# Kernel optimization log

Measured on AMD Instinct MI355X. Metric: run time of the kernel, lower is better.

The kernel has to match this reference:

```python
import jax, jax.numpy as jnp
from jax import lax
import numpy as np

N, BITS, NCLS = 2048, 64, 100
LAMBDA = 1.0
ALPHA = 1.0


def setup_inputs() -> dict:
    key = jax.random.key(0)
    ku, kl = jax.random.split(key)
    u = jax.random.normal(ku, (N, BITS), dtype=jnp.float32)
    labels = jax.random.randint(kl, (N,), 0, NCLS)
    y = jax.nn.one_hot(labels, NCLS, dtype=jnp.float32)  # [N, C]
    return {"u": u, "y": y}


def reference(u, y):
    # inner_product[i, j] = <u_i, u_j>;  s[i, j] = (y_i . y_j > 0)
    ip = u @ u.T                      # [N, N]
    s = (y @ y.T) > 0                 # [N, N] bool

    def step(carry, xs):
        tot, cnt = carry
        ip_row, s_row = xs            # [N], [N]
        pos = s_row
        neg = ~s_row
        # triple[p, n] = ip[p] - ip[n] - ALPHA, clamped like the original
        T = jnp.clip(ip_row[:, None] - ip_row[None, :] - ALPHA, -100.0, 50.0)
        # -(T - log(1 + exp(T))) = softplus(T) - T
        L = jax.nn.softplus(T) - T    # [N, N]
        pm = (pos[:, None] & neg[None, :]).astype(L.dtype)
        npairs = pm.sum()
        valid = (pos.sum() > 0) & (neg.sum() > 0)
        row_loss = jnp.where(valid, (L * pm).sum() / jnp.maximum(npairs, 1.0), 0.0)
        return (tot + row_loss, cnt + valid.astype(jnp.float32)), None

    (tot, cnt), _ = lax.scan(step, (jnp.float32(0.0), jnp.float32(0.0)), (ip, s))
    loss1 = jnp.where(cnt > 0, tot / jnp.maximum(cnt, 1.0), 0.0)
    loss2 = LAMBDA * jnp.mean((u - jnp.sign(u)) ** 2)
    return loss1 + loss2
```

## Files before the change

kernel.cpp:

```cpp
#include <hip/hip_runtime.h>
#include <hip/hip_bf16.h>
#include <math.h>

#define NROWS 2048
#define BITS  64
#define NCLS  100
#define ALPHA_C  1.0f
#define LAMBDA_C 1.0f
#define ECLAMP   1.0e9f
#define NPMAX    64
#define EPS      20

typedef __bf16 bf16x8 __attribute__((ext_vector_type(8)));
typedef float  floatx4 __attribute__((ext_vector_type(4)));


__device__ __forceinline__ float block_reduce_sum(float v, float* wsum) {
    __syncthreads();
    #pragma unroll
    for (int off = 32; off > 0; off >>= 1) v += __shfl_down(v, off);
    int tid = threadIdx.x;
    if ((tid & 63) == 0) wsum[tid >> 6] = v;
    __syncthreads();
    float r = 0.f;
    if (tid == 0) {
        #pragma unroll
        for (int w = 0; w < 4; ++w) r += wsum[w];
    }
    return r;
}

__device__ __forceinline__ float softplus_mt(float T) {
    return fmaxf(-T, 0.f) + __logf(1.f + __expf(-fabsf(T)));
}


__global__ __launch_bounds__(256) void prep_kernel(const float* __restrict__ u,
                                                   const float* __restrict__ y,
                                                   unsigned short* __restrict__ ub,
                                                   unsigned char* __restrict__ lab8,
                                                   float* __restrict__ qp,
                                                   float* __restrict__ rl) {
    const int tid = threadIdx.x;
    if (blockIdx.x < 64) {
        __shared__ float wsum[4];
        const int base = blockIdx.x * 2048 + tid * 8;
        float4 v0 = *(const float4*)(u + base);
        float4 v1 = *(const float4*)(u + base + 4);
        float vv[8] = {v0.x, v0.y, v0.z, v0.w, v1.x, v1.y, v1.z, v1.w};
        unsigned short ob[8];
        float q = 0.f;
        #pragma unroll
        for (int m = 0; m < 8; ++m) {
            const float v = vv[m];
            const float sg = (v > 0.f) ? 1.f : ((v < 0.f) ? -1.f : 0.f);
            const float d = v - sg;
            q = fmaf(d, d, q);
            __hip_bfloat16 h = __float2bfloat16(v);
            ob[m] = *reinterpret_cast<unsigned short*>(&h);
        }
        *(uint4*)(ub + base) = *(const uint4*)ob;
        float t = block_reduce_sum(q, wsum);
        if (tid == 0) qp[blockIdx.x] = t;
    } else {
        const int bi = blockIdx.x - 64;
        if (tid == 0) ((float4*)rl)[bi] = make_float4(0.f, 0.f, 0.f, 0.f);
        const int row = bi * 4 + (tid >> 6);
        const int lane = tid & 63;
        const float* yr = y + (size_t)row * NCLS;
        float v0 = yr[lane];
        float v1 = (lane < NCLS - 64) ? yr[lane + 64] : 0.f;
        unsigned long long m0 = __ballot(v0 > 0.5f);
        unsigned long long m1 = __ballot(v1 > 0.5f);
        if (lane == 0) {
            int c = m0 ? (__ffsll(m0) - 1) : (m1 ? 64 + __ffsll(m1) - 1 : 0);
            lab8[row] = (unsigned char)c;
        }
    }
}

__global__ __launch_bounds__(256) void posk_kernel(const float* __restrict__ u,
                                                   const unsigned char* __restrict__ lab8,
                                                   float* __restrict__ Ep,
                                                   int* __restrict__ npg) {
    __shared__ unsigned char labL[NROWS];
    __shared__ float uloc[4][BITS];
    __shared__ int   lstJ[4][NPMAX];
    const int tid = threadIdx.x;
    const int wave = tid >> 6;
    const int lane = tid & 63;
    const int row = blockIdx.x * 4 + wave;

    ((uint2*)labL)[tid] = ((const uint2*)lab8)[tid];
    uloc[wave][lane] = u[(size_t)row * BITS + lane];
    __syncthreads();

    const int ci = labL[row];
    int np = 0;
    const unsigned long long mylt = (lane == 63) ? ~0ull >> 1
                                                 : ((1ull << (lane + 1)) - 1) >> 1;
    #pragma unroll 4
    for (int m = 0; m < NROWS / 64; ++m) {
        const int j = m * 64 + lane;
        const bool match = (labL[j] == ci);
        unsigned long long bal = __ballot(match);
        if (bal) {
            if (match) {
                const unsigned long long below = (lane == 0) ? 0ull : (bal << (64 - lane));
                const int slot = np + __popcll(below);
                if (slot < NPMAX) lstJ[wave][slot] = j;
            }
            np += __popcll(bal);
        }
    }
    const int npc = (np < NPMAX) ? np : NPMAX;

    float val = 0.f;
    if (lane < npc) {
        const int j = lstJ[wave][lane];
        const float4* uj4 = (const float4*)(u + (size_t)j * BITS);
        float s0 = 0.f, s1 = 0.f, s2 = 0.f, s3 = 0.f;
        #pragma unroll
        for (int kk = 0; kk < BITS / 4; ++kk) {
            float4 vj = uj4[kk];
            s0 = fmaf(vj.x, uloc[wave][4 * kk + 0], s0);
            s1 = fmaf(vj.y, uloc[wave][4 * kk + 1], s1);
            s2 = fmaf(vj.z, uloc[wave][4 * kk + 2], s2);
            s3 = fmaf(vj.w, uloc[wave][4 * kk + 3], s3);
        }
        val = fminf(__expf(-((s0 + s1) + (s2 + s3))), ECLAMP);
    }
    Ep[(size_t)row * NPMAX + lane] = val;
    if (lane == 0) npg[row] = np;
}

__global__ __launch_bounds__(256, 4) void evalj2_kernel(const unsigned short* __restrict__ ub,
                                                        const unsigned char* __restrict__ lab8,
                                                        const float* __restrict__ Ep,
                                                        const int* __restrict__ npg,
                                                        float* __restrict__ rl) {
    __shared__ unsigned char labL[NROWS];
    __shared__ float epT[NPMAX][EPS];
    __shared__ int np16[16];
    __shared__ float wsum[16][4];

    const int tid  = threadIdx.x;
    const int wave = tid >> 6;
    const int lane = tid & 63;
    const int rsel = lane & 15;
    const int quad = lane >> 4;
    const int koff = quad * 8;
    const int i0    = (blockIdx.x >> 3) * 16;
    const int jbase = (blockIdx.x & 7) * 256;

    ((uint2*)labL)[tid] = ((const uint2*)lab8)[tid];
    #pragma unroll
    for (int it = 0; it < 4; ++it) {
        const int idx = tid + it * 256;
        const int r = idx >> 6, k = idx & 63;
        epT[k][r] = Ep[(size_t)(i0 + r) * NPMAX + k];
    }
    if (tid < 16) np16[tid] = npg[i0 + tid];

    uint4 a0r = *(const uint4*)(ub + (size_t)(i0 + rsel) * BITS + koff);
    uint4 a1r = *(const uint4*)(ub + (size_t)(i0 + rsel) * BITS + 32 + koff);
    bf16x8 A0 = __builtin_bit_cast(bf16x8, a0r);
    bf16x8 A1 = __builtin_bit_cast(bf16x8, a1r);

    float Eb[4][4];
    int colj[4];
    #pragma unroll
    for (int t = 0; t < 4; ++t) {
        const int j0 = jbase + (wave * 4 + t) * 16;
        const int jr = j0 + rsel;
        colj[t] = jr;
        uint4 b0r = *(const uint4*)(ub + (size_t)jr * BITS + koff);
        uint4 b1r = *(const uint4*)(ub + (size_t)jr * BITS + 32 + koff);
        bf16x8 B0 = __builtin_bit_cast(bf16x8, b0r);
        bf16x8 B1 = __builtin_bit_cast(bf16x8, b1r);
        floatx4 c = {0.f, 0.f, 0.f, 0.f};
        c = __builtin_amdgcn_mfma_f32_16x16x32_bf16(A0, B0, c, 0, 0, 0);
        c = __builtin_amdgcn_mfma_f32_16x16x32_bf16(A1, B1, c, 0, 0, 0);
        #pragma unroll
        for (int r = 0; r < 4; ++r) {
            const int rowLab = labL[i0 + 4 * quad + r];
            const int colLab = labL[jr];
            Eb[t][r] = (colLab == rowLab) ? 0.f
                                          : fminf(__expf(c[r] + ALPHA_C), ECLAMP);
        }
    }
    __syncthreads();

    int npmx = 0;
    #pragma unroll
    for (int r = 0; r < 16; ++r) {
        int n = np16[r]; n = (n > NPMAX) ? NPMAX : n;
        npmx = (n > npmx) ? n : npmx;
    }
    const int npr = (npmx + 1) & ~1;

    float s[4] = {0.f, 0.f, 0.f, 0.f};
    for (int k = 0; k < npr; k += 2) {
        const float4 e0 = *(const float4*)(&epT[k][4 * quad]);
        const float4 e1 = *(const float4*)(&epT[k + 1][4 * quad]);
        const float e0v[4] = {e0.x, e0.y, e0.z, e0.w};
        const float e1v[4] = {e1.x, e1.y, e1.z, e1.w};
        #pragma unroll
        for (int t = 0; t < 4; ++t) {
            #pragma unroll
            for (int r = 0; r < 4; ++r) {
                const float q0 = Eb[t][r];
                const float f = fmaf(q0, e0v[r], 1.f);
                const float g = fmaf(q0, e1v[r], 1.f);
                s[r] += __log2f(f * g);
            }
        }
    }

    #pragma unroll
    for (int r = 0; r < 4; ++r) {
        #pragma unroll
        for (int off = 1; off < 16; off <<= 1) s[r] += __shfl_xor(s[r], off);
    }
    if (rsel == 0) {
        #pragma unroll
        for (int r = 0; r < 4; ++r) wsum[4 * quad + r][wave] = s[r];
    }
    __syncthreads();
    if (tid < 16) {
        const float ln2 = 0.6931471805599453f;
        const float tot = ((wsum[tid][0] + wsum[tid][1]) +
                           (wsum[tid][2] + wsum[tid][3])) * ln2;
        atomicAdd(&rl[i0 + tid], tot);
    }
}

__global__ __launch_bounds__(256) void finalize3_kernel(const float* __restrict__ rl,
                                                        const int* __restrict__ npg,
                                                        const float* __restrict__ qp,
                                                        float* __restrict__ out) {
    __shared__ float wsum[4];
    const int tid = threadIdx.x;
    float t = 0.f, v = 0.f;
    for (int row = tid; row < NROWS; row += 256) {
        const int np = npg[row];
        const int nneg = NROWS - np;
        const int valid = (np > 0 && nneg > 0) ? 1 : 0;
        t += valid ? (rl[row] / fmaxf((float)np * (float)nneg, 1.f)) : 0.f;
        v += (float)valid;
    }
    float q = (tid < 64) ? qp[tid] : 0.f;
    float tt = block_reduce_sum(t, wsum);
    float vv = block_reduce_sum(v, wsum);
    float qq = block_reduce_sum(q, wsum);
    if (tid == 0) {
        const float loss1 = (vv > 0.f) ? (tt / fmaxf(vv, 1.f)) : 0.f;
        const float loss2 = LAMBDA_C * (qq / (float)(NROWS * BITS));
        out[0] = loss1 + loss2;
    }
}


__global__ __launch_bounds__(256) void labels_only_kernel(const float* __restrict__ y,
                                                          int* __restrict__ labels) {
    const int tid = threadIdx.x;
    const int row = blockIdx.x * 4 + (tid >> 6);
    const int lane = tid & 63;
    const float* yr = y + (size_t)row * NCLS;
    float v0 = yr[lane];
    float v1 = (lane < NCLS - 64) ? yr[lane + 64] : 0.f;
    unsigned long long m0 = __ballot(v0 > 0.5f);
    unsigned long long m1 = __ballot(v1 > 0.5f);
    if (lane == 0) {
        int c = m0 ? (__ffsll(m0) - 1) : (m1 ? 64 + __ffsll(m1) - 1 : 0);
        labels[row] = c;
    }
}

__global__ __launch_bounds__(256) void row_loss_kernel(const float* __restrict__ u,
                                                       const int* __restrict__ labels,
                                                       float* __restrict__ acc) {
    __shared__ float a[NROWS];
    __shared__ float apv[NROWS];
    __shared__ int lab[NROWS];
    __shared__ float ui[BITS];
    __shared__ int npos_s;
    __shared__ float wsum[4];

    const int i = blockIdx.x;
    const int tid = threadIdx.x;

    if (tid < BITS) ui[tid] = u[(size_t)i * BITS + tid];
    if (tid == 0) npos_s = 0;
    __syncthreads();

    #pragma unroll
    for (int m = 0; m < NROWS / 256; ++m) {
        const int j = tid + m * 256;
        const float4* uj = (const float4*)(u + (size_t)j * BITS);
        float s0 = 0.f, s1 = 0.f, s2 = 0.f, s3 = 0.f;
        #pragma unroll
        for (int q = 0; q < BITS / 4; ++q) {
            float4 v = uj[q];
            s0 = fmaf(v.x, ui[4 * q + 0], s0);
            s1 = fmaf(v.y, ui[4 * q + 1], s1);
            s2 = fmaf(v.z, ui[4 * q + 2], s2);
            s3 = fmaf(v.w, ui[4 * q + 3], s3);
        }
        a[j] = (s0 + s1) + (s2 + s3);
        lab[j] = labels[j];
    }
    __syncthreads();

    const int c = lab[i];
    #pragma unroll
    for (int m = 0; m < NROWS / 256; ++m) {
        const int j = tid + m * 256;
        if (lab[j] == c) { int k = atomicAdd(&npos_s, 1); apv[k] = a[j]; }
    }
    __syncthreads();
    const int npos = npos_s;
    const int nneg = NROWS - npos;

    float b[NROWS / 256];
    #pragma unroll
    for (int m = 0; m < NROWS / 256; ++m) {
        const int j = tid + m * 256;
        b[m] = (lab[j] != c) ? (a[j] + ALPHA_C) : -3.0e38f;
    }

    float lsum = 0.f;
    for (int k = 0; k < npos; ++k) {
        const float apk = apv[k];
        #pragma unroll
        for (int m = 0; m < NROWS / 256; ++m) lsum += softplus_mt(apk - b[m]);
    }

    float tot = block_reduce_sum(lsum, wsum);
    if (tid == 0) {
        const int valid = (npos > 0 && nneg > 0) ? 1 : 0;
        const float npairs = fmaxf((float)npos * (float)nneg, 1.f);
        const float rlv = valid ? (tot / npairs) : 0.f;
        atomicAdd(&acc[0], rlv);
        atomicAdd(&acc[1], (float)valid);
    }
}

__global__ __launch_bounds__(256) void quant_kernel(const float* __restrict__ u,
                                                    float* __restrict__ acc) {
    __shared__ float wsum[4];
    const int stride = gridDim.x * 256;
    float s = 0.f;
    for (int t = blockIdx.x * 256 + threadIdx.x; t < NROWS * BITS; t += stride) {
        float v = u[t];
        float sg = (v > 0.f) ? 1.f : ((v < 0.f) ? -1.f : 0.f);
        float d = v - sg;
        s = fmaf(d, d, s);
    }
    float tot = block_reduce_sum(s, wsum);
    if (threadIdx.x == 0) atomicAdd(&acc[2], tot);
}

__global__ void finalize_kernel(const float* __restrict__ acc,
                                float* __restrict__ out) {
    const float tot = acc[0], cnt = acc[1], q = acc[2];
    const float loss1 = (cnt > 0.f) ? (tot / fmaxf(cnt, 1.f)) : 0.f;
    const float loss2 = LAMBDA_C * (q / (float)(NROWS * BITS));
    out[0] = loss1 + loss2;
}


extern "C" void kernel_launch(void* const* d_in, const int* in_sizes, int n_in,
                              void* d_out, int out_size, void* d_ws, size_t ws_size,
                              hipStream_t stream) {
    const float* u = (const float*)d_in[0];
    const float* y = (const float*)d_in[1];
    float* out = (float*)d_out;

    unsigned char* lab8 = (unsigned char*)d_ws;
    float* rl  = (float*)((char*)d_ws + 8192);
    int*   npg = (int*)((char*)d_ws + 16384);
    float* qp  = (float*)((char*)d_ws + 24576);
    float* Ep  = (float*)((char*)d_ws + 32768);
    unsigned short* ub = (unsigned short*)((char*)d_ws + 557056);
    const size_t NEED = 557056 + (size_t)NROWS * BITS * sizeof(unsigned short);

    if (ws_size >= NEED) {
        prep_kernel<<<576, 256, 0, stream>>>(u, y, ub, lab8, qp, rl);
        posk_kernel<<<512, 256, 0, stream>>>(u, lab8, Ep, npg);
        evalj2_kernel<<<1024, 256, 0, stream>>>(ub, lab8, Ep, npg, rl);
        finalize3_kernel<<<1, 256, 0, stream>>>(rl, npg, qp, out);
    } else {
        float* acc2 = (float*)d_ws;
        int*   lab2 = (int*)((char*)d_ws + 256);
        hipMemsetAsync(d_ws, 0, 256, stream);
        labels_only_kernel<<<512, 256, 0, stream>>>(y, lab2);
        row_loss_kernel<<<NROWS, 256, 0, stream>>>(u, lab2, acc2);
        quant_kernel<<<64, 256, 0, stream>>>(u, acc2);
        finalize_kernel<<<1, 1, 0, stream>>>(acc2, out);
    }
}
```

Before: 81.16 us.

## Fuse finalize into eval kernel via last-block atomic counter

Removes the separate single-block finalize launch by having the last-finishing block of the eval kernel, detected with a global atomic counter reset in the prep kernel, compute the final loss. Launch bounds are also raised to allow more resident blocks per CU. This cuts one kernel launch and its inter-kernel gap, at the cost of an extra atomic and threadfence per block and a serial tail in one block.

Result: slower. 91.29 us (+12.5%).

```diff
diff --git a/kernel.cpp b/kernel.cpp
--- a/kernel.cpp
+++ b/kernel.cpp
@@ -40,7 +40,8 @@
                                                    unsigned short* __restrict__ ub,
                                                    unsigned char* __restrict__ lab8,
                                                    float* __restrict__ qp,
-                                                   float* __restrict__ rl) {
+                                                   float* __restrict__ rl,
+                                                   unsigned int* __restrict__ counter) {
     const int tid = threadIdx.x;
     if (blockIdx.x < 64) {
         __shared__ float wsum[4];
@@ -64,7 +65,10 @@
         if (tid == 0) qp[blockIdx.x] = t;
     } else {
         const int bi = blockIdx.x - 64;
-        if (tid == 0) ((float4*)rl)[bi] = make_float4(0.f, 0.f, 0.f, 0.f);
+        if (tid == 0) {
+            ((float4*)rl)[bi] = make_float4(0.f, 0.f, 0.f, 0.f);
+            if (bi == 0) *counter = 0u;
+        }
         const int row = bi * 4 + (tid >> 6);
         const int lane = tid & 63;
         const float* yr = y + (size_t)row * NCLS;
@@ -97,8 +101,6 @@
 
     const int ci = labL[row];
     int np = 0;
-    const unsigned long long mylt = (lane == 63) ? ~0ull >> 1
-                                                 : ((1ull << (lane + 1)) - 1) >> 1;
     #pragma unroll 4
     for (int m = 0; m < NROWS / 64; ++m) {
         const int j = m * 64 + lane;
@@ -134,15 +136,20 @@
     if (lane == 0) npg[row] = np;
 }
 
-__global__ __launch_bounds__(256, 4) void evalj2_kernel(const unsigned short* __restrict__ ub,
+__global__ __launch_bounds__(256, 6) void evalj3_kernel(const unsigned short* __restrict__ ub,
                                                         const unsigned char* __restrict__ lab8,
                                                         const float* __restrict__ Ep,
                                                         const int* __restrict__ npg,
-                                                        float* __restrict__ rl) {
+                                                        const float* __restrict__ qp,
+                                                        float* __restrict__ rl,
+                                                        unsigned int* __restrict__ counter,
+                                                        float* __restrict__ out) {
     __shared__ unsigned char labL[NROWS];
-    __shared__ float epT[NPMAX][EPS];
+    alignas(16) __shared__ float epT[NPMAX][EPS];
     __shared__ int np16[16];
-    __shared__ float wsum[16][4];
+    __shared__ float wsum16[16][4];
+    __shared__ float wsumA[4];
+    __shared__ int lastFlag;
 
     const int tid  = threadIdx.x;
     const int wave = tid >> 6;
@@ -168,12 +175,9 @@
     bf16x8 A1 = __builtin_bit_cast(bf16x8, a1r);
 
     float Eb[4][4];
-    int colj[4];
     #pragma unroll
     for (int t = 0; t < 4; ++t) {
-        const int j0 = jbase + (wave * 4 + t) * 16;
-        const int jr = j0 + rsel;
-        colj[t] = jr;
+        const int jr = jbase + (wave * 4 + t) * 16 + rsel;
         uint4 b0r = *(const uint4*)(ub + (size_t)jr * BITS + koff);
         uint4 b1r = *(const uint4*)(ub + (size_t)jr * BITS + 32 + koff);
         bf16x8 B0 = __builtin_bit_cast(bf16x8, b0r);
@@ -224,39 +228,40 @@
     }
     if (rsel == 0) {
         #pragma unroll
-        for (int r = 0; r < 4; ++r) wsum[4 * quad + r][wave] = s[r];
+        for (int r = 0; r < 4; ++r) wsum16[4 * quad + r][wave] = s[r];
     }
     __syncthreads();
     if (tid < 16) {
         const float ln2 = 0.6931471805599453f;
-        const float tot = ((wsum[tid][0] + wsum[tid][1]) +
-                           (wsum[tid][2] + wsum[tid][3])) * ln2;
+        const float tot = ((wsum16[tid][0] + wsum16[tid][1]) +
+                           (wsum16[tid][2] + wsum16[tid][3])) * ln2;
         atomicAdd(&rl[i0 + tid], tot);
     }
-}
-
-__global__ __launch_bounds__(256) void finalize3_kernel(const float* __restrict__ rl,
-                                                        const int* __restrict__ npg,
-                                                        const float* __restrict__ qp,
-                                                        float* __restrict__ out) {
-    __shared__ float wsum[4];
-    const int tid = threadIdx.x;
-    float t = 0.f, v = 0.f;
-    for (int row = tid; row < NROWS; row += 256) {
-        const int np = npg[row];
-        const int nneg = NROWS - np;
-        const int valid = (np > 0 && nneg > 0) ? 1 : 0;
-        t += valid ? (rl[row] / fmaxf((float)np * (float)nneg, 1.f)) : 0.f;
-        v += (float)valid;
-    }
-    float q = (tid < 64) ? qp[tid] : 0.f;
-    float tt = block_reduce_sum(t, wsum);
-    float vv = block_reduce_sum(v, wsum);
-    float qq = block_reduce_sum(q, wsum);
     if (tid == 0) {
-        const float loss1 = (vv > 0.f) ? (tt / fmaxf(vv, 1.f)) : 0.f;
-        const float loss2 = LAMBDA_C * (qq / (float)(NROWS * BITS));
-        out[0] = loss1 + loss2;
+        __threadfence();
+        unsigned int old = atomicAdd(counter, 1u);
+        lastFlag = (old == (unsigned int)(gridDim.x - 1)) ? 1 : 0;
+    }
+    __syncthreads();
+    if (lastFlag) {
+        float t = 0.f, v = 0.f;
+        for (int row = tid; row < NROWS; row += 256) {
+            const int np = npg[row];
+            const int nneg = NROWS - np;
+            const int valid = (np > 0 && nneg > 0) ? 1 : 0;
+            const float rv = atomicAdd(&rl[row], 0.f);
+            t += valid ? (rv / fmaxf((float)np * (float)nneg, 1.f)) : 0.f;
+            v += (float)valid;
+        }
+        float q = (tid < 64) ? qp[tid] : 0.f;
+        float tt = block_reduce_sum(t, wsumA);
+        float vv = block_reduce_sum(v, wsumA);
+        float qq = block_reduce_sum(q, wsumA);
+        if (tid == 0) {
+            const float loss1 = (vv > 0.f) ? (tt / fmaxf(vv, 1.f)) : 0.f;
+            const float loss2 = LAMBDA_C * (qq / (float)(NROWS * BITS));
+            out[0] = loss1 + loss2;
+        }
     }
 }
 
@@ -322,18 +327,18 @@
     const int npos = npos_s;
     const int nneg = NROWS - npos;
 
-    float b[NROWS / 256];
+    float bb[NROWS / 256];
     #pragma unroll
     for (int m = 0; m < NROWS / 256; ++m) {
         const int j = tid + m * 256;
-        b[m] = (lab[j] != c) ? (a[j] + ALPHA_C) : -3.0e38f;
+        bb[m] = (lab[j] != c) ? (a[j] + ALPHA_C) : -3.0e38f;
     }
 
     float lsum = 0.f;
     for (int k = 0; k < npos; ++k) {
         const float apk = apv[k];
         #pragma unroll
-        for (int m = 0; m < NROWS / 256; ++m) lsum += softplus_mt(apk - b[m]);
+        for (int m = 0; m < NROWS / 256; ++m) lsum += softplus_mt(apk - bb[m]);
     }
 
     float tot = block_reduce_sum(lsum, wsum);
@@ -381,15 +386,15 @@
     float* rl  = (float*)((char*)d_ws + 8192);
     int*   npg = (int*)((char*)d_ws + 16384);
     float* qp  = (float*)((char*)d_ws + 24576);
+    unsigned int* counter = (unsigned int*)((char*)d_ws + 24832);
     float* Ep  = (float*)((char*)d_ws + 32768);
     unsigned short* ub = (unsigned short*)((char*)d_ws + 557056);
     const size_t NEED = 557056 + (size_t)NROWS * BITS * sizeof(unsigned short);
 
     if (ws_size >= NEED) {
-        prep_kernel<<<576, 256, 0, stream>>>(u, y, ub, lab8, qp, rl);
+        prep_kernel<<<576, 256, 0, stream>>>(u, y, ub, lab8, qp, rl, counter);
         posk_kernel<<<512, 256, 0, stream>>>(u, lab8, Ep, npg);
-        evalj2_kernel<<<1024, 256, 0, stream>>>(ub, lab8, Ep, npg, rl);
-        finalize3_kernel<<<1, 256, 0, stream>>>(rl, npg, qp, out);
+        evalj3_kernel<<<1024, 256, 0, stream>>>(ub, lab8, Ep, npg, qp, rl, counter, out);
     } else {
         float* acc2 = (float*)d_ws;
         int*   lab2 = (int*)((char*)d_ws + 256);
```
